# Performance work log

Measured on AMD Instinct MI355X. Metric: run time of the kernel, lower is better.

## Reference

```python
import jax, jax.numpy as jnp
import numpy as np

NUM_HEADS = 16


def setup_inputs() -> dict:
    key = jax.random.key(0)
    ks = jax.random.split(key, 6)
    B, N, L, C = 2, 1024, 4096, 1024
    x_obj = jax.random.normal(ks[0], (B, N, C), dtype=jnp.float32)
    x_ctx = jax.random.normal(ks[1], (B, L, C), dtype=jnp.float32)
    s = 1.0 / np.sqrt(C)
    Wq = jax.random.normal(ks[2], (C, C), dtype=jnp.float32) * s
    Wkv = jax.random.normal(ks[3], (C, 2 * C), dtype=jnp.float32) * s
    Wproj = jax.random.normal(ks[4], (C, C), dtype=jnp.float32) * s
    bproj = jax.random.normal(ks[5], (C,), dtype=jnp.float32) * 0.01
    return {"x_obj": x_obj, "x_ctx": x_ctx, "Wq": Wq, "Wkv": Wkv,
            "Wproj": Wproj, "bproj": bproj}


def _split_heads(t, H):
    # [B, T, C] -> [B, H, T, d]
    B, T, C = t.shape
    return t.reshape(B, T, H, C // H).transpose(0, 2, 1, 3)


def reference(x_obj, x_ctx, Wq, Wkv, Wproj, bproj):
    B, N, C = x_obj.shape
    H = NUM_HEADS
    d = C // H
    scale = d ** -0.5

    q = _split_heads(x_obj @ Wq, H)                      # [B,H,N,d]

    kv_o = x_obj @ Wkv                                   # [B,N,2C] -> (2,H,d) split
    k_obj = _split_heads(kv_o[..., :C], H)               # [B,H,N,d]
    v_obj = _split_heads(kv_o[..., C:], H)

    kv_c = x_ctx @ Wkv                                   # [B,L,2C]
    k_ctx = _split_heads(kv_c[..., :C], H)               # [B,H,L,d]
    v_ctx = _split_heads(kv_c[..., C:], H)

    k = jnp.concatenate([k_obj, k_ctx], axis=2)          # [B,H,N+L,d]
    v = jnp.concatenate([v_obj, v_ctx], axis=2)

    attn = jnp.einsum('bhnd,bhmd->bhnm', q, k) * scale   # [B,H,N,N+L]
    attn = jax.nn.softmax(attn, axis=-1)
    out = jnp.einsum('bhnm,bhmd->bhnd', attn, v)         # [B,H,N,d]
    out = out.transpose(0, 2, 1, 3).reshape(B, N, C)
    return out @ Wproj + bproj
```

## Files before the change

kernel.cpp:

```cpp
#include <hip/hip_runtime.h>
#include <stdint.h>

typedef unsigned short u16;
typedef unsigned int   u32;
typedef __attribute__((ext_vector_type(8))) short bf16x8;
typedef __attribute__((ext_vector_type(4))) float f32x4;

__device__ __forceinline__ u16 f2bf(float f) {
    union { float f; u32 u; } v; v.f = f;
    return (u16)((v.u + 0x7FFFu + ((v.u >> 16) & 1u)) >> 16);
}
__device__ __forceinline__ float bf2f(u16 h) {
    union { u32 u; float f; } v; v.u = ((u32)h) << 16; return v.f;
}

__device__ __forceinline__ void async16(const u16* g, u16* l) {
    typedef __attribute__((address_space(1))) const u32 gq;
    typedef __attribute__((address_space(3))) u32 lq;
    __builtin_amdgcn_global_load_lds((gq*)g, (lq*)l, 16, 0, 0);
}

__global__ void cvt_cat_k(const float* __restrict__ xo, const float* __restrict__ xc,
                          u16* __restrict__ Xc)
{
    int t = blockIdx.x * 256 + threadIdx.x;
    int row = t >> 8, cid = (t & 255) * 4;
    int b = row >= 5120, s = row - b * 5120;
    const float* src = (s < 1024)
        ? xo + ((size_t)(b * 1024 + s)) * 1024 + cid
        : xc + ((size_t)(b * 4096 + s - 1024)) * 1024 + cid;
    float4 f = *(const float4*)src;
    union { u16 a[4]; uint2 v; } p;
    p.a[0] = f2bf(f.x); p.a[1] = f2bf(f.y); p.a[2] = f2bf(f.z); p.a[3] = f2bf(f.w);
    *(uint2*)(Xc + (size_t)row * 1024 + cid) = p.v;
}

__global__ void cvt_t_k(const float* __restrict__ W, u16* __restrict__ Wt,
                        int N, int K)
{
    __shared__ __align__(16) u16 Ts[64][72];
    int t = threadIdx.x;
    int n0 = blockIdx.x * 64, k0 = blockIdx.y * 64;
    int lr = t >> 2, lc = (t & 3) * 16;
    const float* src = W + (size_t)(k0 + lr) * N + n0 + lc;
    union { u16 a[8]; uint4 v; } p0, p1;
    float4 f0 = *(const float4*)(src),      f1 = *(const float4*)(src + 4);
    float4 f2 = *(const float4*)(src + 8),  f3 = *(const float4*)(src + 12);
    p0.a[0]=f2bf(f0.x); p0.a[1]=f2bf(f0.y); p0.a[2]=f2bf(f0.z); p0.a[3]=f2bf(f0.w);
    p0.a[4]=f2bf(f1.x); p0.a[5]=f2bf(f1.y); p0.a[6]=f2bf(f1.z); p0.a[7]=f2bf(f1.w);
    p1.a[0]=f2bf(f2.x); p1.a[1]=f2bf(f2.y); p1.a[2]=f2bf(f2.z); p1.a[3]=f2bf(f2.w);
    p1.a[4]=f2bf(f3.x); p1.a[5]=f2bf(f3.y); p1.a[6]=f2bf(f3.z); p1.a[7]=f2bf(f3.w);
    *(uint4*)&Ts[lr][lc]     = p0.v;
    *(uint4*)&Ts[lr][lc + 8] = p1.v;
    __syncthreads();
    union { u16 a[8]; uint4 v; } q0, q1;
#pragma unroll
    for (int j = 0; j < 8; ++j) q0.a[j] = Ts[lc + j][lr];
#pragma unroll
    for (int j = 0; j < 8; ++j) q1.a[j] = Ts[lc + 8 + j][lr];
    u16* dst = Wt + (size_t)(n0 + lr) * K + k0 + lc;
    *(uint4*)dst       = q0.v;
    *(uint4*)(dst + 8) = q1.v;
}

template<int AMAP, int EPI, int BN>
__global__ __launch_bounds__(256, 2)
void gemm_bt(const u16* __restrict__ A, const u16* __restrict__ Bt,
             const float* __restrict__ bias, u16* __restrict__ C,
             float* __restrict__ Cf, u16* __restrict__ Kh, u16* __restrict__ Vh,
             int M, int N, int K)
{
    __shared__ __align__(16) u16 As[128 * 32];
    __shared__ __align__(16) u16 Bs[BN * 32];

    const int t = threadIdx.x, w = t >> 6;
    const int lane = t & 63, quad = lane >> 4, l16 = lane & 15;
    const int m0 = blockIdx.y * 128, n0 = blockIdx.x * BN;
    const int wr = (BN == 128) ? (w >> 1) * 64 : w * 32;
    const int wc = (BN == 128) ? (w & 1) * 64 : 0;
    constexpr int MI = (BN == 128) ? 4 : 2;

    const int sr0 = w * 32 + (lane >> 2), sr1 = sr0 + 16;
    const int cg  = (lane & 3) ^ ((lane >> 4) & 3);
    u16* abase = As + w * 1024;
    u16* bbase = Bs + w * ((BN == 128) ? 1024 : 512);

    const u16 *ar0, *ar1;
    {
        int g0 = m0 + sr0, g1 = m0 + sr1;
        if (AMAP == 1) {
            ar0 = A + ((size_t)(g0 >> 10) * 5120 + (g0 & 1023)) * 1024;
            ar1 = A + ((size_t)(g1 >> 10) * 5120 + (g1 & 1023)) * 1024;
        } else {
            ar0 = A + (size_t)g0 * 1024;
            ar1 = A + (size_t)g1 * 1024;
        }
        ar0 += cg * 8; ar1 += cg * 8;
    }
    const u16* br0;
    const u16* br1 = nullptr;
    if (BN == 128) {
        br0 = Bt + (size_t)(n0 + sr0) * 1024 + cg * 8;
        br1 = Bt + (size_t)(n0 + sr1) * 1024 + cg * 8;
    } else {
        br0 = Bt + (size_t)(n0 + w * 16 + (lane >> 2)) * 1024 + cg * 8;
    }

    f32x4 acc[MI][4] = {};
    const int sel = (quad ^ (l16 >> 2)) * 8;

    for (int k0 = 0; k0 < K; k0 += 32) {
        async16(ar0 + k0, abase);
        async16(ar1 + k0, abase + 512);
        async16(br0 + k0, bbase);
        if (BN == 128) async16(br1 + k0, bbase + 512);
        __syncthreads();

        bf16x8 av[MI], bv[4];
#pragma unroll
        for (int i = 0; i < MI; ++i)
            av[i] = *(const bf16x8*)&As[(wr + i * 16 + l16) * 32 + sel];
#pragma unroll
        for (int j = 0; j < 4; ++j)
            bv[j] = *(const bf16x8*)&Bs[(wc + j * 16 + l16) * 32 + sel];
#pragma unroll
        for (int i = 0; i < MI; ++i)
#pragma unroll
            for (int j = 0; j < 4; ++j)
                acc[i][j] = __builtin_amdgcn_mfma_f32_16x16x32_bf16(av[i], bv[j], acc[i][j], 0, 0, 0);
        __syncthreads();
    }

#pragma unroll
    for (int j = 0; j < 4; ++j) {
        int col = n0 + wc + j * 16 + l16;
#pragma unroll
        for (int i = 0; i < MI; ++i) {
            int rowb = m0 + wr + i * 16 + quad * 4;
            if (EPI == 0) {
#pragma unroll
                for (int r = 0; r < 4; ++r)
                    C[(size_t)(rowb + r) * N + col] = f2bf(acc[i][j][r]);
            } else if (EPI == 2) {
                float bvl = bias[col];
#pragma unroll
                for (int r = 0; r < 4; ++r)
                    Cf[(size_t)(rowb + r) * N + col] = acc[i][j][r] + bvl;
            } else {
                int b = rowb >= 5120;
                int key = rowb - b * 5120;
                if (col < 1024) {
                    int bh = b * 16 + (col >> 6), d = col & 63;
                    u16* dst = Kh + ((size_t)bh * 5120 + key) * 64 + d;
#pragma unroll
                    for (int r = 0; r < 4; ++r) dst[r * 64] = f2bf(acc[i][j][r]);
                } else {
                    int c2 = col - 1024;
                    int bh = b * 16 + (c2 >> 6), d = c2 & 63;
                    union { u16 a[4]; uint2 v; } pk;
#pragma unroll
                    for (int r = 0; r < 4; ++r) pk.a[r] = f2bf(acc[i][j][r]);
                    *(uint2*)(Vh + ((size_t)bh * 64 + d) * 5120 + key) = pk.v;
                }
            }
        }
    }
}

__global__ __launch_bounds__(256, 4)
void attn_k(const u16* __restrict__ Q, const u16* __restrict__ Kh,
            const u16* __restrict__ Vh, u16* __restrict__ Op,
            float* __restrict__ Lp)
{
    __shared__ __align__(16) u16 Ks[64][72];
    __shared__ __align__(16) u16 Vt[64][72];
    __shared__ __align__(16) u16 Ps[4][32][72];

    const int tid  = threadIdx.x;
    const int wave = tid >> 6, lane = tid & 63;
    const int quad = lane >> 4, l16 = lane & 15;
    const int bx = blockIdx.x;
    const int part = bx & 3, qt = (bx >> 2) & 7, h = (bx >> 5) & 15, b = bx >> 9;
    const int bh = b * 16 + h;

    const int qrow0 = b * 1024 + qt * 128 + wave * 32;
    const u16* qbase = Q + (size_t)qrow0 * 1024 + h * 64;

    bf16x8 aq[2][2];
#pragma unroll
    for (int rt = 0; rt < 2; ++rt) {
        aq[rt][0] = *(const bf16x8*)(qbase + (size_t)(rt * 16 + l16) * 1024 +      quad * 8);
        aq[rt][1] = *(const bf16x8*)(qbase + (size_t)(rt * 16 + l16) * 1024 + 32 + quad * 8);
    }

    f32x4 o[2][4] = {};
    f32x4 lv[2] = {};

    const u16* kbase = Kh + (size_t)bh * 5120 * 64;
    const u16* vbase = Vh + (size_t)bh * 64 * 5120;
    const int skey = tid >> 2, sdc = (tid & 3) * 16;
    const int m_beg = part * 1280;

    for (int c = 0; c < 20; ++c) {
        const int m0 = m_beg + c * 64;
        {
            const u16* src = kbase + (size_t)(m0 + skey) * 64 + sdc;
            *(uint4*)&Ks[skey][sdc]     = *(const uint4*)(src);
            *(uint4*)&Ks[skey][sdc + 8] = *(const uint4*)(src + 8);
        }
        {
            const u16* vsrc = vbase + (size_t)skey * 5120 + m0 + sdc;
            *(uint4*)&Vt[skey][sdc]     = *(const uint4*)(vsrc);
            *(uint4*)&Vt[skey][sdc + 8] = *(const uint4*)(vsrc + 8);
        }
        __syncthreads();

        f32x4 s[2][4] = {};
#pragma unroll
        for (int nt = 0; nt < 4; ++nt) {
            bf16x8 kb0 = *(const bf16x8*)&Ks[nt * 16 + l16][     quad * 8];
            bf16x8 kb1 = *(const bf16x8*)&Ks[nt * 16 + l16][32 + quad * 8];
#pragma unroll
            for (int rt = 0; rt < 2; ++rt) {
                s[rt][nt] = __builtin_amdgcn_mfma_f32_16x16x32_bf16(aq[rt][0], kb0, s[rt][nt], 0, 0, 0);
                s[rt][nt] = __builtin_amdgcn_mfma_f32_16x16x32_bf16(aq[rt][1], kb1, s[rt][nt], 0, 0, 0);
            }
        }

#pragma unroll
        for (int rt = 0; rt < 2; ++rt)
#pragma unroll
            for (int nt = 0; nt < 4; ++nt)
#pragma unroll
                for (int r = 0; r < 4; ++r) {
                    float e = __expf(s[rt][nt][r] * 0.125f);
                    lv[rt][r] += e;
                    Ps[wave][rt * 16 + quad * 4 + r][nt * 16 + l16] = f2bf(e);
                }

        asm volatile("s_waitcnt lgkmcnt(0)" ::: "memory");

        bf16x8 pf[2][2];
#pragma unroll
        for (int rt = 0; rt < 2; ++rt) {
            pf[rt][0] = *(const bf16x8*)&Ps[wave][rt * 16 + l16][     quad * 8];
            pf[rt][1] = *(const bf16x8*)&Ps[wave][rt * 16 + l16][32 + quad * 8];
        }

#pragma unroll
        for (int dt = 0; dt < 4; ++dt) {
            bf16x8 v0 = *(const bf16x8*)&Vt[dt * 16 + l16][     quad * 8];
            bf16x8 v1 = *(const bf16x8*)&Vt[dt * 16 + l16][32 + quad * 8];
#pragma unroll
            for (int rt = 0; rt < 2; ++rt) {
                o[rt][dt] = __builtin_amdgcn_mfma_f32_16x16x32_bf16(pf[rt][0], v0, o[rt][dt], 0, 0, 0);
                o[rt][dt] = __builtin_amdgcn_mfma_f32_16x16x32_bf16(pf[rt][1], v1, o[rt][dt], 0, 0, 0);
            }
        }
        __syncthreads();
    }

    float lsum[2][4];
#pragma unroll
    for (int rt = 0; rt < 2; ++rt)
#pragma unroll
        for (int r = 0; r < 4; ++r) {
            float x = lv[rt][r];
#pragma unroll
            for (int off = 8; off >= 1; off >>= 1)
                x += __shfl_xor(x, off, 64);
            lsum[rt][r] = x;
        }

    const int Rb = bh * 1024 + qt * 128 + wave * 32;
    u16* obase = Op + ((size_t)part << 21);
#pragma unroll
    for (int rt = 0; rt < 2; ++rt)
#pragma unroll
        for (int dt = 0; dt < 4; ++dt)
#pragma unroll
            for (int r = 0; r < 4; ++r) {
                int R = Rb + rt * 16 + quad * 4 + r;
                obase[(size_t)R * 64 + dt * 16 + l16] = f2bf(o[rt][dt][r]);
            }
    if (l16 == 0) {
#pragma unroll
        for (int rt = 0; rt < 2; ++rt)
#pragma unroll
            for (int r = 0; r < 4; ++r)
                Lp[part * 32768 + Rb + rt * 16 + quad * 4 + r] = lsum[rt][r];
    }
}

__global__ void comb_k(const u16* __restrict__ Op, const float* __restrict__ Lp,
                       u16* __restrict__ ao)
{
    int t = blockIdx.x * 256 + threadIdx.x;
    int R = t >> 4, dg = (t & 15) * 4;
    float l = Lp[R] + Lp[32768 + R] + Lp[65536 + R] + Lp[98304 + R];
    float a[4] = {0.f, 0.f, 0.f, 0.f};
#pragma unroll
    for (int p = 0; p < 4; ++p) {
        union { u16 a[4]; uint2 v; } w;
        w.v = *(const uint2*)(Op + ((size_t)p << 21) + (size_t)R * 64 + dg);
#pragma unroll
        for (int j = 0; j < 4; ++j) a[j] += bf2f(w.a[j]);
    }
    float inv = 1.f / l;
    int bh = R >> 10, n = R & 1023, b = bh >> 4, h = bh & 15;
    union { u16 a[4]; uint2 v; } out;
#pragma unroll
    for (int j = 0; j < 4; ++j) out.a[j] = f2bf(a[j] * inv);
    *(uint2*)(ao + (size_t)(b * 1024 + n) * 1024 + h * 64 + dg) = out.v;
}

extern "C" void kernel_launch(void* const* d_in, const int* in_sizes, int n_in,
                              void* d_out, int out_size, void* d_ws, size_t ws_size,
                              hipStream_t stream)
{
    const float* x_obj = (const float*)d_in[0];
    const float* x_ctx = (const float*)d_in[1];
    const float* Wq    = (const float*)d_in[2];
    const float* Wkv   = (const float*)d_in[3];
    const float* Wproj = (const float*)d_in[4];
    const float* bproj = (const float*)d_in[5];
    float* out = (float*)d_out;

    u16* Xc  = (u16*)d_ws;
    u16* ao  = Xc;
    u16* Op  = Xc + (size_t)2097152;
    u16* Wqt = Xc  + (size_t)10485760;
    u16* Wkt = Wqt + (size_t)1048576;
    u16* Wpt = Wkt + (size_t)2097152;
    u16* q   = Wpt + (size_t)1048576;
    u16* Kh  = q   + (size_t)2097152;
    u16* Vh  = Kh  + (size_t)10485760;
    float* Lp = (float*)(Vh + (size_t)10485760);

    dim3 blk(256);
    cvt_cat_k<<<dim3(10240), blk, 0, stream>>>(x_obj, x_ctx, Xc);
    cvt_t_k<<<dim3(16, 16), blk, 0, stream>>>(Wq,    Wqt, 1024, 1024);
    cvt_t_k<<<dim3(32, 16), blk, 0, stream>>>(Wkv,   Wkt, 2048, 1024);
    cvt_t_k<<<dim3(16, 16), blk, 0, stream>>>(Wproj, Wpt, 1024, 1024);

    gemm_bt<1, 0, 64><<<dim3(16, 16), blk, 0, stream>>>(
        Xc, Wqt, nullptr, q, nullptr, nullptr, nullptr, 2048, 1024, 1024);
    gemm_bt<0, 1, 128><<<dim3(16, 80), blk, 0, stream>>>(
        Xc, Wkt, nullptr, nullptr, nullptr, Kh, Vh, 10240, 2048, 1024);
    attn_k<<<dim3(1024), blk, 0, stream>>>(q, Kh, Vh, Op, Lp);
    comb_k<<<dim3(2048), blk, 0, stream>>>(Op, Lp, ao);
    gemm_bt<0, 2, 64><<<dim3(16, 16), blk, 0, stream>>>(
        ao, Wpt, bproj, nullptr, out, nullptr, nullptr, 2048, 1024, 1024);
}
```

Before: 281.4 us.

## Use 32x32x16 MFMA in attention with register-resident P and merged weight conversion

Attention now uses 32x32x16 bf16 MFMA tiles with S computed transposed (K as the A operand), so the exponentiated probabilities stay in registers. They are packed to bf16 with a byte permute and exchanged across half-waves with shuffles instead of going through a shared-memory P buffer, which drops LDS traffic and a wait. exp is rewritten as exp2f with the log2e factor folded into the scale. The three weight convert-transpose launches are merged into one kernel to cut launch overhead. The risk is more register pressure and the cost of the cross-lane shuffles.

```diff
diff --git a/kernel.cpp b/kernel.cpp
--- a/kernel.cpp
+++ b/kernel.cpp
@@ -5,6 +5,7 @@
 typedef unsigned int   u32;
 typedef __attribute__((ext_vector_type(8))) short bf16x8;
 typedef __attribute__((ext_vector_type(4))) float f32x4;
+typedef __attribute__((ext_vector_type(16))) float f32x16;
 
 __device__ __forceinline__ u16 f2bf(float f) {
     union { float f; u32 u; } v; v.f = f;
@@ -12,6 +13,9 @@
 }
 __device__ __forceinline__ float bf2f(u16 h) {
     union { u32 u; float f; } v; v.u = ((u32)h) << 16; return v.f;
+}
+__device__ __forceinline__ u32 fbits(float f) {
+    union { float f; u32 u; } v; v.f = f; return v.u;
 }
 
 __device__ __forceinline__ void async16(const u16* g, u16* l) {
@@ -35,12 +39,21 @@
     *(uint2*)(Xc + (size_t)row * 1024 + cid) = p.v;
 }
 
-__global__ void cvt_t_k(const float* __restrict__ W, u16* __restrict__ Wt,
-                        int N, int K)
+__global__ void cvt_w_k(const float* __restrict__ Wq, const float* __restrict__ Wkv,
+                        const float* __restrict__ Wp,
+                        u16* __restrict__ Wqt, u16* __restrict__ Wkt,
+                        u16* __restrict__ Wpt)
 {
     __shared__ __align__(16) u16 Ts[64][72];
+    int id = blockIdx.x;
+    const float* W; u16* Wt; int N, tile;
+    if (id < 256)      { W = Wq;  Wt = Wqt; N = 1024; tile = id; }
+    else if (id < 768) { W = Wkv; Wt = Wkt; N = 2048; tile = id - 256; }
+    else               { W = Wp;  Wt = Wpt; N = 1024; tile = id - 768; }
+    int nt = N >> 6;
+    int n0 = (tile % nt) * 64, k0 = (tile / nt) * 64;
+
     int t = threadIdx.x;
-    int n0 = blockIdx.x * 64, k0 = blockIdx.y * 64;
     int lr = t >> 2, lc = (t & 3) * 16;
     const float* src = W + (size_t)(k0 + lr) * N + n0 + lc;
     union { u16 a[8]; uint4 v; } p0, p1;
@@ -58,7 +71,7 @@
     for (int j = 0; j < 8; ++j) q0.a[j] = Ts[lc + j][lr];
 #pragma unroll
     for (int j = 0; j < 8; ++j) q1.a[j] = Ts[lc + 8 + j][lr];
-    u16* dst = Wt + (size_t)(n0 + lr) * K + k0 + lc;
+    u16* dst = Wt + (size_t)(n0 + lr) * 1024 + k0 + lc;
     *(uint4*)dst       = q0.v;
     *(uint4*)(dst + 8) = q1.v;
 }
@@ -174,32 +187,30 @@
 {
     __shared__ __align__(16) u16 Ks[64][72];
     __shared__ __align__(16) u16 Vt[64][72];
-    __shared__ __align__(16) u16 Ps[4][32][72];
 
     const int tid  = threadIdx.x;
     const int wave = tid >> 6, lane = tid & 63;
-    const int quad = lane >> 4, l16 = lane & 15;
+    const int n31 = lane & 31, H = lane >> 5;
     const int bx = blockIdx.x;
     const int part = bx & 3, qt = (bx >> 2) & 7, h = (bx >> 5) & 15, b = bx >> 9;
     const int bh = b * 16 + h;
 
     const int qrow0 = b * 1024 + qt * 128 + wave * 32;
-    const u16* qbase = Q + (size_t)qrow0 * 1024 + h * 64;
-
-    bf16x8 aq[2][2];
-#pragma unroll
-    for (int rt = 0; rt < 2; ++rt) {
-        aq[rt][0] = *(const bf16x8*)(qbase + (size_t)(rt * 16 + l16) * 1024 +      quad * 8);
-        aq[rt][1] = *(const bf16x8*)(qbase + (size_t)(rt * 16 + l16) * 1024 + 32 + quad * 8);
-    }
-
-    f32x4 o[2][4] = {};
-    f32x4 lv[2] = {};
+    const u16* qbase = Q + (size_t)(qrow0 + n31) * 1024 + h * 64;
+
+    bf16x8 aq[4];
+#pragma unroll
+    for (int ks = 0; ks < 4; ++ks)
+        aq[ks] = *(const bf16x8*)(qbase + ks * 16 + H * 8);
+
+    f32x16 o[2] = {};
+    float lv = 0.f;
 
     const u16* kbase = Kh + (size_t)bh * 5120 * 64;
     const u16* vbase = Vh + (size_t)bh * 64 * 5120;
     const int skey = tid >> 2, sdc = (tid & 3) * 16;
     const int m_beg = part * 1280;
+    const float SC = 0.18033688f;
 
     for (int c = 0; c < 20; ++c) {
         const int m0 = m_beg + c * 64;
@@ -215,81 +226,63 @@
         }
         __syncthreads();
 
-        f32x4 s[2][4] = {};
-#pragma unroll
-        for (int nt = 0; nt < 4; ++nt) {
-            bf16x8 kb0 = *(const bf16x8*)&Ks[nt * 16 + l16][     quad * 8];
-            bf16x8 kb1 = *(const bf16x8*)&Ks[nt * 16 + l16][32 + quad * 8];
-#pragma unroll
-            for (int rt = 0; rt < 2; ++rt) {
-                s[rt][nt] = __builtin_amdgcn_mfma_f32_16x16x32_bf16(aq[rt][0], kb0, s[rt][nt], 0, 0, 0);
-                s[rt][nt] = __builtin_amdgcn_mfma_f32_16x16x32_bf16(aq[rt][1], kb1, s[rt][nt], 0, 0, 0);
+        u32 pk[2][8];
+#pragma unroll
+        for (int kt = 0; kt < 2; ++kt) {
+            f32x16 s = {};
+#pragma unroll
+            for (int ks = 0; ks < 4; ++ks) {
+                bf16x8 ka = *(const bf16x8*)&Ks[kt * 32 + n31][ks * 16 + H * 8];
+                s = __builtin_amdgcn_mfma_f32_32x32x16_bf16(ka, aq[ks], s, 0, 0, 0);
             }
-        }
-
-#pragma unroll
-        for (int rt = 0; rt < 2; ++rt)
-#pragma unroll
-            for (int nt = 0; nt < 4; ++nt)
-#pragma unroll
-                for (int r = 0; r < 4; ++r) {
-                    float e = __expf(s[rt][nt][r] * 0.125f);
-                    lv[rt][r] += e;
-                    Ps[wave][rt * 16 + quad * 4 + r][nt * 16 + l16] = f2bf(e);
+#pragma unroll
+            for (int i = 0; i < 8; ++i) {
+                float e0 = exp2f(s[2 * i]     * SC);
+                float e1 = exp2f(s[2 * i + 1] * SC);
+                lv += e0 + e1;
+                pk[kt][i] = __builtin_amdgcn_perm(fbits(e1), fbits(e0), 0x07060302u);
+            }
+        }
+
+#pragma unroll
+        for (int kt = 0; kt < 2; ++kt)
+#pragma unroll
+            for (int kp = 0; kp < 2; ++kp) {
+                u32 oA = H ? pk[kt][4 * kp + 2] : pk[kt][4 * kp];
+                u32 oB = H ? pk[kt][4 * kp + 3] : pk[kt][4 * kp + 1];
+                u32 pA = H ? pk[kt][4 * kp]     : pk[kt][4 * kp + 2];
+                u32 pB = H ? pk[kt][4 * kp + 1] : pk[kt][4 * kp + 3];
+                u32 rA = __shfl_xor((int)pA, 32, 64);
+                u32 rB = __shfl_xor((int)pB, 32, 64);
+                union { u32 u[4]; bf16x8 v; } bb;
+                bb.u[0] = H ? rA : oA;
+                bb.u[1] = H ? rB : oB;
+                bb.u[2] = H ? oA : rA;
+                bb.u[3] = H ? oB : rB;
+#pragma unroll
+                for (int dt = 0; dt < 2; ++dt) {
+                    bf16x8 va = *(const bf16x8*)&Vt[dt * 32 + n31][kt * 32 + kp * 16 + H * 8];
+                    o[dt] = __builtin_amdgcn_mfma_f32_32x32x16_bf16(va, bb.v, o[dt], 0, 0, 0);
                 }
-
-        asm volatile("s_waitcnt lgkmcnt(0)" ::: "memory");
-
-        bf16x8 pf[2][2];
-#pragma unroll
-        for (int rt = 0; rt < 2; ++rt) {
-            pf[rt][0] = *(const bf16x8*)&Ps[wave][rt * 16 + l16][     quad * 8];
-            pf[rt][1] = *(const bf16x8*)&Ps[wave][rt * 16 + l16][32 + quad * 8];
-        }
-
-#pragma unroll
-        for (int dt = 0; dt < 4; ++dt) {
-            bf16x8 v0 = *(const bf16x8*)&Vt[dt * 16 + l16][     quad * 8];
-            bf16x8 v1 = *(const bf16x8*)&Vt[dt * 16 + l16][32 + quad * 8];
-#pragma unroll
-            for (int rt = 0; rt < 2; ++rt) {
-                o[rt][dt] = __builtin_amdgcn_mfma_f32_16x16x32_bf16(pf[rt][0], v0, o[rt][dt], 0, 0, 0);
-                o[rt][dt] = __builtin_amdgcn_mfma_f32_16x16x32_bf16(pf[rt][1], v1, o[rt][dt], 0, 0, 0);
             }
-        }
         __syncthreads();
     }
 
-    float lsum[2][4];
-#pragma unroll
-    for (int rt = 0; rt < 2; ++rt)
-#pragma unroll
-        for (int r = 0; r < 4; ++r) {
-            float x = lv[rt][r];
-#pragma unroll
-            for (int off = 8; off >= 1; off >>= 1)
-                x += __shfl_xor(x, off, 64);
-            lsum[rt][r] = x;
-        }
-
-    const int Rb = bh * 1024 + qt * 128 + wave * 32;
-    u16* obase = Op + ((size_t)part << 21);
-#pragma unroll
-    for (int rt = 0; rt < 2; ++rt)
-#pragma unroll
-        for (int dt = 0; dt < 4; ++dt)
-#pragma unroll
-            for (int r = 0; r < 4; ++r) {
-                int R = Rb + rt * 16 + quad * 4 + r;
-                obase[(size_t)R * 64 + dt * 16 + l16] = f2bf(o[rt][dt][r]);
-            }
-    if (l16 == 0) {
-#pragma unroll
-        for (int rt = 0; rt < 2; ++rt)
-#pragma unroll
-            for (int r = 0; r < 4; ++r)
-                Lp[part * 32768 + Rb + rt * 16 + quad * 4 + r] = lsum[rt][r];
-    }
+    float lf = lv + __shfl_xor(lv, 32, 64);
+
+    const int R = bh * 1024 + qt * 128 + wave * 32 + n31;
+    u16* obase = Op + ((size_t)part << 21) + (size_t)R * 64;
+#pragma unroll
+    for (int dt = 0; dt < 2; ++dt)
+#pragma unroll
+        for (int g = 0; g < 4; ++g) {
+            union { u16 a[4]; uint2 v; } pkv;
+#pragma unroll
+            for (int r = 0; r < 4; ++r) pkv.a[r] = f2bf(o[dt][4 * g + r]);
+            *(uint2*)(obase + dt * 32 + 8 * g + 4 * H) = pkv.v;
+        }
+    if (H == 0)
+        Lp[part * 32768 + R] = lf;
 }
 
 __global__ void comb_k(const u16* __restrict__ Op, const float* __restrict__ Lp,
@@ -339,9 +332,7 @@
 
     dim3 blk(256);
     cvt_cat_k<<<dim3(10240), blk, 0, stream>>>(x_obj, x_ctx, Xc);
-    cvt_t_k<<<dim3(16, 16), blk, 0, stream>>>(Wq,    Wqt, 1024, 1024);
-    cvt_t_k<<<dim3(32, 16), blk, 0, stream>>>(Wkv,   Wkt, 2048, 1024);
-    cvt_t_k<<<dim3(16, 16), blk, 0, stream>>>(Wproj, Wpt, 1024, 1024);
+    cvt_w_k<<<dim3(1024), blk, 0, stream>>>(Wq, Wkv, Wproj, Wqt, Wkt, Wpt);
 
     gemm_bt<1, 0, 64><<<dim3(16, 16), blk, 0, stream>>>(
         Xc, Wqt, nullptr, q, nullptr, nullptr, nullptr, 2048, 1024, 1024);
```

New measurement: 294.4 us. 4.6% more time.

## Merge weight conversions and Q/KV GEMMs into single launches, stage V transpose via LDS

Applied to the files above, without the earlier changes.

Folds the three weight transpose/convert launches into one kernel that picks the matrix by block index. Folds the Q projection into the KV GEMM launch as extra 128x128 tiles, removing a launch and filling the GPU with one larger grid. The V epilogue now writes through a shared-memory transpose so Vh is stored with 16-byte coalesced writes instead of scattered 8-byte stores. Shared memory per block grows to hold the transpose buffer, which may reduce occupancy.

```diff
diff --git a/kernel.cpp b/kernel.cpp
--- a/kernel.cpp
+++ b/kernel.cpp
@@ -35,12 +35,21 @@
     *(uint2*)(Xc + (size_t)row * 1024 + cid) = p.v;
 }
 
-__global__ void cvt_t_k(const float* __restrict__ W, u16* __restrict__ Wt,
-                        int N, int K)
+__global__ void cvt_w_k(const float* __restrict__ Wq, const float* __restrict__ Wkv,
+                        const float* __restrict__ Wp,
+                        u16* __restrict__ Wqt, u16* __restrict__ Wkt,
+                        u16* __restrict__ Wpt)
 {
     __shared__ __align__(16) u16 Ts[64][72];
+    int id = blockIdx.x;
+    const float* W; u16* Wt; int N, tile;
+    if (id < 256)      { W = Wq;  Wt = Wqt; N = 1024; tile = id; }
+    else if (id < 768) { W = Wkv; Wt = Wkt; N = 2048; tile = id - 256; }
+    else               { W = Wp;  Wt = Wpt; N = 1024; tile = id - 768; }
+    int nt = N >> 6;
+    int n0 = (tile % nt) * 64, k0 = (tile / nt) * 64;
+
     int t = threadIdx.x;
-    int n0 = blockIdx.x * 64, k0 = blockIdx.y * 64;
     int lr = t >> 2, lc = (t & 3) * 16;
     const float* src = W + (size_t)(k0 + lr) * N + n0 + lc;
     union { u16 a[8]; uint4 v; } p0, p1;
@@ -58,37 +67,38 @@
     for (int j = 0; j < 8; ++j) q0.a[j] = Ts[lc + j][lr];
 #pragma unroll
     for (int j = 0; j < 8; ++j) q1.a[j] = Ts[lc + 8 + j][lr];
-    u16* dst = Wt + (size_t)(n0 + lr) * K + k0 + lc;
+    u16* dst = Wt + (size_t)(n0 + lr) * 1024 + k0 + lc;
     *(uint4*)dst       = q0.v;
     *(uint4*)(dst + 8) = q1.v;
 }
 
-template<int AMAP, int EPI, int BN>
 __global__ __launch_bounds__(256, 2)
-void gemm_bt(const u16* __restrict__ A, const u16* __restrict__ Bt,
-             const float* __restrict__ bias, u16* __restrict__ C,
-             float* __restrict__ Cf, u16* __restrict__ Kh, u16* __restrict__ Vh,
-             int M, int N, int K)
-{
-    __shared__ __align__(16) u16 As[128 * 32];
-    __shared__ __align__(16) u16 Bs[BN * 32];
+void gemm_qkv(const u16* __restrict__ A, const u16* __restrict__ Wqt,
+              const u16* __restrict__ Wkt, u16* __restrict__ q,
+              u16* __restrict__ Kh, u16* __restrict__ Vh)
+{
+    __shared__ __align__(16) u16 smem[17408];
+    u16* As = smem;
+    u16* Bs = smem + 4096;
 
     const int t = threadIdx.x, w = t >> 6;
     const int lane = t & 63, quad = lane >> 4, l16 = lane & 15;
-    const int m0 = blockIdx.y * 128, n0 = blockIdx.x * BN;
-    const int wr = (BN == 128) ? (w >> 1) * 64 : w * 32;
-    const int wc = (BN == 128) ? (w & 1) * 64 : 0;
-    constexpr int MI = (BN == 128) ? 4 : 2;
+    const int id = blockIdx.x;
+    const bool qm = id >= 1280;
+    int m0, n0; const u16* Bt;
+    if (qm) { int t2 = id - 1280; m0 = (t2 >> 3) * 128; n0 = (t2 & 7) * 128; Bt = Wqt; }
+    else    { m0 = (id >> 4) * 128; n0 = (id & 15) * 128; Bt = Wkt; }
+    const int wr = (w >> 1) * 64, wc = (w & 1) * 64;
 
     const int sr0 = w * 32 + (lane >> 2), sr1 = sr0 + 16;
     const int cg  = (lane & 3) ^ ((lane >> 4) & 3);
     u16* abase = As + w * 1024;
-    u16* bbase = Bs + w * ((BN == 128) ? 1024 : 512);
+    u16* bbase = Bs + w * 1024;
 
     const u16 *ar0, *ar1;
     {
         int g0 = m0 + sr0, g1 = m0 + sr1;
-        if (AMAP == 1) {
+        if (qm) {
             ar0 = A + ((size_t)(g0 >> 10) * 5120 + (g0 & 1023)) * 1024;
             ar1 = A + ((size_t)(g1 >> 10) * 5120 + (g1 & 1023)) * 1024;
         } else {
@@ -97,72 +107,145 @@
         }
         ar0 += cg * 8; ar1 += cg * 8;
     }
-    const u16* br0;
-    const u16* br1 = nullptr;
-    if (BN == 128) {
-        br0 = Bt + (size_t)(n0 + sr0) * 1024 + cg * 8;
-        br1 = Bt + (size_t)(n0 + sr1) * 1024 + cg * 8;
-    } else {
-        br0 = Bt + (size_t)(n0 + w * 16 + (lane >> 2)) * 1024 + cg * 8;
-    }
-
-    f32x4 acc[MI][4] = {};
+    const u16* br0 = Bt + (size_t)(n0 + sr0) * 1024 + cg * 8;
+    const u16* br1 = Bt + (size_t)(n0 + sr1) * 1024 + cg * 8;
+
+    f32x4 acc[4][4] = {};
     const int sel = (quad ^ (l16 >> 2)) * 8;
 
-    for (int k0 = 0; k0 < K; k0 += 32) {
+    for (int k0 = 0; k0 < 1024; k0 += 32) {
         async16(ar0 + k0, abase);
         async16(ar1 + k0, abase + 512);
         async16(br0 + k0, bbase);
-        if (BN == 128) async16(br1 + k0, bbase + 512);
-        __syncthreads();
-
-        bf16x8 av[MI], bv[4];
-#pragma unroll
-        for (int i = 0; i < MI; ++i)
+        async16(br1 + k0, bbase + 512);
+        __syncthreads();
+
+        bf16x8 av[4], bv[4];
+#pragma unroll
+        for (int i = 0; i < 4; ++i)
             av[i] = *(const bf16x8*)&As[(wr + i * 16 + l16) * 32 + sel];
 #pragma unroll
         for (int j = 0; j < 4; ++j)
             bv[j] = *(const bf16x8*)&Bs[(wc + j * 16 + l16) * 32 + sel];
 #pragma unroll
-        for (int i = 0; i < MI; ++i)
+        for (int i = 0; i < 4; ++i)
 #pragma unroll
             for (int j = 0; j < 4; ++j)
                 acc[i][j] = __builtin_amdgcn_mfma_f32_16x16x32_bf16(av[i], bv[j], acc[i][j], 0, 0, 0);
         __syncthreads();
     }
 
+    if (qm) {
+#pragma unroll
+        for (int j = 0; j < 4; ++j) {
+            int col = n0 + wc + j * 16 + l16;
+#pragma unroll
+            for (int i = 0; i < 4; ++i) {
+                int rowb = m0 + wr + i * 16 + quad * 4;
+#pragma unroll
+                for (int r = 0; r < 4; ++r)
+                    q[(size_t)(rowb + r) * 1024 + col] = f2bf(acc[i][j][r]);
+            }
+        }
+    } else if (n0 < 1024) {
+#pragma unroll
+        for (int j = 0; j < 4; ++j) {
+            int col = n0 + wc + j * 16 + l16;
+#pragma unroll
+            for (int i = 0; i < 4; ++i) {
+                int rowb = m0 + wr + i * 16 + quad * 4;
+                int b = rowb >= 5120;
+                int key = rowb - b * 5120;
+                int bh = b * 16 + (col >> 6), d = col & 63;
+                u16* dst = Kh + ((size_t)bh * 5120 + key) * 64 + d;
+#pragma unroll
+                for (int r = 0; r < 4; ++r) dst[r * 64] = f2bf(acc[i][j][r]);
+            }
+        }
+    } else {
+        u16* Tv = smem;
+#pragma unroll
+        for (int j = 0; j < 4; ++j) {
+            int d2 = wc + j * 16 + l16;
+#pragma unroll
+            for (int i = 0; i < 4; ++i) {
+                int kl = wr + i * 16 + quad * 4;
+                union { u16 a[4]; uint2 v; } pk;
+#pragma unroll
+                for (int r = 0; r < 4; ++r) pk.a[r] = f2bf(acc[i][j][r]);
+                *(uint2*)&Tv[d2 * 136 + kl] = pk.v;
+            }
+        }
+        __syncthreads();
+        int b = m0 >= 5120;
+        int keyb = m0 - b * 5120;
+        int hb = (n0 - 1024) >> 6;
+#pragma unroll
+        for (int p = 0; p < 8; ++p) {
+            int idx = p * 256 + t;
+            int d2 = idx >> 4, k0c = (idx & 15) * 8;
+            uint4 vv = *(const uint4*)&Tv[d2 * 136 + k0c];
+            int bh = b * 16 + hb + (d2 >> 6), d = d2 & 63;
+            *(uint4*)(Vh + ((size_t)bh * 64 + d) * 5120 + keyb + k0c) = vv;
+        }
+    }
+}
+
+__global__ __launch_bounds__(256, 2)
+void gemm_proj(const u16* __restrict__ A, const u16* __restrict__ Bt,
+               const float* __restrict__ bias, float* __restrict__ Cf)
+{
+    __shared__ __align__(16) u16 As[128 * 32];
+    __shared__ __align__(16) u16 Bs[64 * 32];
+
+    const int t = threadIdx.x, w = t >> 6;
+    const int lane = t & 63, quad = lane >> 4, l16 = lane & 15;
+    const int m0 = blockIdx.y * 128, n0 = blockIdx.x * 64;
+    const int wr = w * 32, wc = 0;
+
+    const int sr0 = w * 32 + (lane >> 2), sr1 = sr0 + 16;
+    const int cg  = (lane & 3) ^ ((lane >> 4) & 3);
+    u16* abase = As + w * 1024;
+    u16* bbase = Bs + w * 512;
+
+    const u16* ar0 = A + (size_t)(m0 + sr0) * 1024 + cg * 8;
+    const u16* ar1 = A + (size_t)(m0 + sr1) * 1024 + cg * 8;
+    const u16* br0 = Bt + (size_t)(n0 + w * 16 + (lane >> 2)) * 1024 + cg * 8;
+
+    f32x4 acc[2][4] = {};
+    const int sel = (quad ^ (l16 >> 2)) * 8;
+
+    for (int k0 = 0; k0 < 1024; k0 += 32) {
+        async16(ar0 + k0, abase);
+        async16(ar1 + k0, abase + 512);
+        async16(br0 + k0, bbase);
+        __syncthreads();
+
+        bf16x8 av[2], bv[4];
+#pragma unroll
+        for (int i = 0; i < 2; ++i)
+            av[i] = *(const bf16x8*)&As[(wr + i * 16 + l16) * 32 + sel];
+#pragma unroll
+        for (int j = 0; j < 4; ++j)
+            bv[j] = *(const bf16x8*)&Bs[(wc + j * 16 + l16) * 32 + sel];
+#pragma unroll
+        for (int i = 0; i < 2; ++i)
+#pragma unroll
+            for (int j = 0; j < 4; ++j)
+                acc[i][j] = __builtin_amdgcn_mfma_f32_16x16x32_bf16(av[i], bv[j], acc[i][j], 0, 0, 0);
+        __syncthreads();
+    }
+
 #pragma unroll
     for (int j = 0; j < 4; ++j) {
         int col = n0 + wc + j * 16 + l16;
-#pragma unroll
-        for (int i = 0; i < MI; ++i) {
+        float bvl = bias[col];
+#pragma unroll
+        for (int i = 0; i < 2; ++i) {
             int rowb = m0 + wr + i * 16 + quad * 4;
-            if (EPI == 0) {
-#pragma unroll
-                for (int r = 0; r < 4; ++r)
-                    C[(size_t)(rowb + r) * N + col] = f2bf(acc[i][j][r]);
-            } else if (EPI == 2) {
-                float bvl = bias[col];
-#pragma unroll
-                for (int r = 0; r < 4; ++r)
-                    Cf[(size_t)(rowb + r) * N + col] = acc[i][j][r] + bvl;
-            } else {
-                int b = rowb >= 5120;
-                int key = rowb - b * 5120;
-                if (col < 1024) {
-                    int bh = b * 16 + (col >> 6), d = col & 63;
-                    u16* dst = Kh + ((size_t)bh * 5120 + key) * 64 + d;
-#pragma unroll
-                    for (int r = 0; r < 4; ++r) dst[r * 64] = f2bf(acc[i][j][r]);
-                } else {
-                    int c2 = col - 1024;
-                    int bh = b * 16 + (c2 >> 6), d = c2 & 63;
-                    union { u16 a[4]; uint2 v; } pk;
-#pragma unroll
-                    for (int r = 0; r < 4; ++r) pk.a[r] = f2bf(acc[i][j][r]);
-                    *(uint2*)(Vh + ((size_t)bh * 64 + d) * 5120 + key) = pk.v;
-                }
-            }
+#pragma unroll
+            for (int r = 0; r < 4; ++r)
+                Cf[(size_t)(rowb + r) * 1024 + col] = acc[i][j][r] + bvl;
         }
     }
 }
@@ -339,16 +422,10 @@
 
     dim3 blk(256);
     cvt_cat_k<<<dim3(10240), blk, 0, stream>>>(x_obj, x_ctx, Xc);
-    cvt_t_k<<<dim3(16, 16), blk, 0, stream>>>(Wq,    Wqt, 1024, 1024);
-    cvt_t_k<<<dim3(32, 16), blk, 0, stream>>>(Wkv,   Wkt, 2048, 1024);
-    cvt_t_k<<<dim3(16, 16), blk, 0, stream>>>(Wproj, Wpt, 1024, 1024);
-
-    gemm_bt<1, 0, 64><<<dim3(16, 16), blk, 0, stream>>>(
-        Xc, Wqt, nullptr, q, nullptr, nullptr, nullptr, 2048, 1024, 1024);
-    gemm_bt<0, 1, 128><<<dim3(16, 80), blk, 0, stream>>>(
-        Xc, Wkt, nullptr, nullptr, nullptr, Kh, Vh, 10240, 2048, 1024);
+    cvt_w_k<<<dim3(1024), blk, 0, stream>>>(Wq, Wkv, Wproj, Wqt, Wkt, Wpt);
+
+    gemm_qkv<<<dim3(1408), blk, 0, stream>>>(Xc, Wqt, Wkt, q, Kh, Vh);
     attn_k<<<dim3(1024), blk, 0, stream>>>(q, Kh, Vh, Op, Lp);
     comb_k<<<dim3(2048), blk, 0, stream>>>(Op, Lp, ao);
-    gemm_bt<0, 2, 64><<<dim3(16, 16), blk, 0, stream>>>(
-        ao, Wpt, bproj, nullptr, out, nullptr, nullptr, 2048, 1024, 1024);
-}
+    gemm_proj<<<dim3(16, 16), blk, 0, stream>>>(ao, Wpt, bproj, out);
+}
```

Result: faster. 255.7 us (-9.1%).
